# Optimization experiments

Measured on AMD Instinct MI355X. Metric: run time of the kernel, lower is better.

Reference implementation:

```python
import jax, jax.numpy as jnp
import numpy as np

N_NODES = 100000
N_EDGES = 1_600_000
IN, HID, OUT = 512, 128, 40


def setup_inputs() -> dict:
    key = jax.random.key(0)
    ks = jax.random.split(key, 7)
    features = jax.random.normal(ks[0], (N_NODES, IN), dtype=jnp.float32)
    src = jax.random.randint(ks[1], (N_EDGES,), 0, N_NODES, dtype=jnp.int32)
    dst = jax.random.randint(ks[2], (N_EDGES,), 0, N_NODES, dtype=jnp.int32)
    # Glorot-ish init for GraphConv weights; zero bias (DGL default)
    W1 = jax.random.normal(ks[3], (IN, HID), dtype=jnp.float32) * np.float32(1.0 / np.sqrt(IN))
    b1 = jnp.zeros((HID,), dtype=jnp.float32)
    W2 = jax.random.normal(ks[4], (HID, OUT), dtype=jnp.float32) * np.float32(1.0 / np.sqrt(HID))
    b2 = jnp.zeros((OUT,), dtype=jnp.float32)
    return {"features": features, "src": src, "dst": dst,
            "W1": W1, "b1": b1, "W2": W2, "b2": b2}


def _degree_norms(src, dst, n_nodes):
    ones = jnp.ones(src.shape[0], dtype=jnp.float32)
    deg_out = jax.ops.segment_sum(ones, src, num_segments=n_nodes)
    deg_in = jax.ops.segment_sum(ones, dst, num_segments=n_nodes)
    # DGL clamps degree to min 1 before the -1/2 power
    norm_src = jax.lax.rsqrt(jnp.maximum(deg_out, 1.0))  # [N]
    norm_dst = jax.lax.rsqrt(jnp.maximum(deg_in, 1.0))   # [N]
    return norm_src, norm_dst


def _graph_conv(x, W, b, src, dst, norm_src, norm_dst):
    # norm='both': out = D_dst^{-1/2} A D_src^{-1/2} (x W) + b
    # W applied before aggregation (in_feats > out_feats path in DGL)
    h = (x * norm_src[:, None]) @ W            # [N, out_feats]
    agg = jax.ops.segment_sum(h[src], dst, num_segments=x.shape[0])  # SpMM
    return agg * norm_dst[:, None] + b


def reference(features, src, dst, W1, b1, W2, b2):
    norm_src, norm_dst = _degree_norms(src, dst, features.shape[0])
    h = _graph_conv(features, W1, b1, src, dst, norm_src, norm_dst)
    h = jax.nn.relu(h)
    # dropout1: identity in eval mode
    h = _graph_conv(h, W2, b2, src, dst, norm_src, norm_dst)
    # dropout2: identity in eval mode
    return h
```

## Files before the change

### kernel.cpp

```cpp
#include <hip/hip_runtime.h>
#include <hip/hip_bf16.h>

#define N_NODES 100000
#define N_EDGES 1600000
#define FIN 512
#define FHID 128
#define FOUT 40
#define FOUTP 48

#define SCAN_CHUNK 1024
#define SCAN_NB ((N_NODES + SCAN_CHUNK - 1) / SCAN_CHUNK)

#define NRANGE 8
#define RANGE_SZ 12500
#define GH 16
#define EDGE_SLICE (N_EDGES / GH)

typedef __attribute__((ext_vector_type(8))) short short8;
typedef __attribute__((ext_vector_type(4))) float f32x4;

static __device__ inline unsigned short f2bf(float f) {
    unsigned x = __float_as_uint(f);
    unsigned r = (x + 0x7fffu + ((x >> 16) & 1u)) >> 16;
    return (unsigned short)r;
}

static __device__ inline unsigned pk2bf(float lo, float hi) {
    __hip_bfloat162 h = __float22bfloat162_rn(make_float2(lo, hi));
    return *(unsigned*)&h;
}
static __device__ inline unsigned short bf1(float f) {
    __hip_bfloat16 h = __float2bfloat16(f);
    return *(unsigned short*)&h;
}

static __device__ inline void gload_lds16(const unsigned short* g, unsigned short* l) {
    __builtin_amdgcn_global_load_lds(
        (const __attribute__((address_space(1))) unsigned int*)(g),
        (__attribute__((address_space(3))) unsigned int*)(l), 16, 0, 0);
}

__global__ __launch_bounds__(256) void deg_hist(const int* __restrict__ src,
                                                const int* __restrict__ dst,
                                                unsigned* __restrict__ scratch) {
    __shared__ unsigned hist[RANGE_SZ];
    const int task = blockIdx.x / GH;
    const int g = blockIdx.x % GH;
    const int a = task / NRANGE;
    const int rg = task % NRANGE;
    const int lo = rg * RANGE_SZ;
    const int t = threadIdx.x;
    for (int i = t; i < RANGE_SZ; i += 256) hist[i] = 0;
    __syncthreads();
    const int* arr = a ? dst : src;
    const int4* p = (const int4*)(arr + g * EDGE_SLICE);
    for (int i = t; i < EDGE_SLICE / 4; i += 256) {
        int4 v = p[i];
        int x;
        x = v.x - lo; if ((unsigned)x < RANGE_SZ) atomicAdd(&hist[x], 1u);
        x = v.y - lo; if ((unsigned)x < RANGE_SZ) atomicAdd(&hist[x], 1u);
        x = v.z - lo; if ((unsigned)x < RANGE_SZ) atomicAdd(&hist[x], 1u);
        x = v.w - lo; if ((unsigned)x < RANGE_SZ) atomicAdd(&hist[x], 1u);
    }
    __syncthreads();
    unsigned* out = scratch + ((size_t)task * GH + g) * RANGE_SZ;
    for (int i = t; i < RANGE_SZ; i += 256) out[i] = hist[i];
}

__global__ __launch_bounds__(256) void deg_reduce_scan(const unsigned* __restrict__ scratch,
                                                       float* __restrict__ nsrc,
                                                       float* __restrict__ ndst,
                                                       unsigned* __restrict__ degI,
                                                       unsigned* __restrict__ bsum) {
    __shared__ unsigned red[256];
    const int b = blockIdx.x, t = threadIdx.x;
    unsigned mysum = 0;
#pragma unroll
    for (int i = 0; i < 4; i++) {
        int node = b * SCAN_CHUNK + i * 256 + t;
        if (node < N_NODES) {
            const int rg = node / RANGE_SZ;
            const int off = node % RANGE_SZ;
            const unsigned* ps = scratch + ((size_t)rg * GH) * RANGE_SZ + off;
            const unsigned* pd = scratch + ((size_t)(NRANGE + rg) * GH) * RANGE_SZ + off;
            unsigned so = 0, si = 0;
#pragma unroll
            for (int g = 0; g < GH; g++) {
                so += ps[(size_t)g * RANGE_SZ];
                si += pd[(size_t)g * RANGE_SZ];
            }
            degI[node] = si;
            nsrc[node] = rsqrtf((float)(so < 1u ? 1u : so));
            ndst[node] = rsqrtf((float)(si < 1u ? 1u : si));
            mysum += si;
        }
    }
    red[t] = mysum; __syncthreads();
    for (int off = 128; off > 0; off >>= 1) {
        if (t < off) red[t] += red[t + off];
        __syncthreads();
    }
    if (t == 0) bsum[b] = red[0];
}

__global__ void scan_bsum(unsigned* __restrict__ bsum, int* __restrict__ rowptr) {
    __shared__ unsigned s[128];
    int t = threadIdx.x;
    if (t < SCAN_NB) s[t] = bsum[t];
    __syncthreads();
    if (t == 0) {
        unsigned run = 0;
        for (int i = 0; i < SCAN_NB; i++) { unsigned x = s[i]; s[i] = run; run += x; }
    }
    __syncthreads();
    if (t < SCAN_NB) bsum[t] = s[t];
    if (t == 0) rowptr[N_NODES] = N_EDGES;
}

__global__ __launch_bounds__(256) void scan_write_mk(const unsigned* __restrict__ deg,
                                                     const unsigned* __restrict__ bsum,
                                                     int* __restrict__ rowptr,
                                                     unsigned* __restrict__ scratch) {
    __shared__ unsigned ts[256];
    int b = blockIdx.x, t = threadIdx.x;
    int base = b * SCAN_CHUNK + t * 4;
    unsigned v[4]; unsigned sum = 0;
#pragma unroll
    for (int i = 0; i < 4; i++) { int idx = base + i; v[i] = (idx < N_NODES) ? deg[idx] : 0u; sum += v[i]; }
    ts[t] = sum; __syncthreads();
    for (int off = 1; off < 256; off <<= 1) {
        unsigned add = (t >= off) ? ts[t - off] : 0u;
        __syncthreads();
        ts[t] += add;
        __syncthreads();
    }
    unsigned excl = (t == 0) ? 0u : ts[t - 1];
    unsigned run = bsum[b] + excl;
#pragma unroll
    for (int i = 0; i < 4; i++) {
        int idx = base + i;
        if (idx < N_NODES) {
            rowptr[idx] = (int)run;
            const int rg = idx / RANGE_SZ;
            const int off = idx % RANGE_SZ;
            unsigned* pd = scratch + ((size_t)(NRANGE + rg) * GH) * RANGE_SZ + off;
            unsigned nrun = run;
#pragma unroll
            for (int g = 0; g < GH; g++) {
                unsigned c = pd[(size_t)g * RANGE_SZ];
                pd[(size_t)g * RANGE_SZ] = nrun;
                nrun += c;
            }
        }
        run += v[i];
    }
}

__global__ __launch_bounds__(256) void scatter2(const int* __restrict__ src,
                                                const int* __restrict__ dst,
                                                const unsigned* __restrict__ scratch,
                                                int* __restrict__ esrc) {
    __shared__ unsigned cur[RANGE_SZ];
    const int rg = blockIdx.x / GH;
    const int g = blockIdx.x % GH;
    const int lo = rg * RANGE_SZ;
    const int t = threadIdx.x;
    const unsigned* base = scratch + ((size_t)(NRANGE + rg) * GH + g) * RANGE_SZ;
    for (int i = t; i < RANGE_SZ; i += 256) cur[i] = base[i];
    __syncthreads();
    const int4* pd = (const int4*)(dst + g * EDGE_SLICE);
    const int4* ps = (const int4*)(src + g * EDGE_SLICE);
    for (int i = t; i < EDGE_SLICE / 4; i += 256) {
        int4 d4 = pd[i];
        int4 s4 = ps[i];
        int x;
        x = d4.x - lo; if ((unsigned)x < RANGE_SZ) esrc[atomicAdd(&cur[x], 1u)] = s4.x;
        x = d4.y - lo; if ((unsigned)x < RANGE_SZ) esrc[atomicAdd(&cur[x], 1u)] = s4.y;
        x = d4.z - lo; if ((unsigned)x < RANGE_SZ) esrc[atomicAdd(&cur[x], 1u)] = s4.z;
        x = d4.w - lo; if ((unsigned)x < RANGE_SZ) esrc[atomicAdd(&cur[x], 1u)] = s4.w;
    }
}

__global__ __launch_bounds__(256) void wcvt_all(const float* __restrict__ W1,
                                                const float* __restrict__ W2,
                                                unsigned short* __restrict__ Wt,
                                                unsigned short* __restrict__ W2t) {
    int j = blockIdx.x * blockDim.x + threadIdx.x;
    if (j < FIN * FHID) {
        int k = j >> 7;
        int n = j & 127;
        Wt[n * FIN + k] = f2bf(W1[j]);
    } else if (j < FIN * FHID + FOUTP * FHID) {
        int jj = j - FIN * FHID;
        int n = jj >> 7;
        int k = jj & 127;
        W2t[jj] = (n < FOUT) ? f2bf(W2[k * FOUT + n]) : (unsigned short)0;
    }
}

__global__ __launch_bounds__(256) void gemm1_mfma(const float* __restrict__ X,
                                                  const unsigned short* __restrict__ Wt,
                                                  const float* __restrict__ nsrc,
                                                  unsigned short* __restrict__ H) {
    __shared__ __align__(16) unsigned short Xs[64 * 64];
    __shared__ __align__(16) unsigned short Bs[128 * 64];
    const int t = threadIdx.x;
    const int bm = blockIdx.x * 64;
    const int w = t >> 6;
    const int l = t & 63;
    const int r = l & 15;
    const int kg = l >> 4;

    f32x4 acc[8];
#pragma unroll
    for (int c = 0; c < 8; c++) acc[c] = (f32x4){0.f, 0.f, 0.f, 0.f};

    for (int s = 0; s < FIN / 64; ++s) {
        const int k0 = s * 64;
#pragma unroll
        for (int i = 0; i < 4; i++) {
            int c = i * 4 + w;
            int col = c * 8 + (l >> 3);
            int slotp = l & 7;
            gload_lds16(Wt + (size_t)col * FIN + k0 + ((slotp ^ (col & 7)) * 8),
                        Bs + c * 512);
        }
#pragma unroll
        for (int i = 0; i < 2; i++) {
            int idx = t + i * 256;
            int row = idx >> 3;
            int slot = idx & 7;
            int grow = bm + row;
            uint4 packed = make_uint4(0u, 0u, 0u, 0u);
            if (grow < N_NODES) {
                const float4* p = (const float4*)(X + (size_t)grow * FIN + k0 + slot * 8);
                float4 v0 = p[0];
                float4 v1 = p[1];
                packed.x = pk2bf(v0.x, v0.y);
                packed.y = pk2bf(v0.z, v0.w);
                packed.z = pk2bf(v1.x, v1.y);
                packed.w = pk2bf(v1.z, v1.w);
            }
            *(uint4*)&Xs[row * 64 + ((slot ^ (row & 7)) * 8)] = packed;
        }
        __syncthreads();
        const int arow = w * 16 + r;
        short8 a0 = *(const short8*)&Xs[arow * 64 + (((0 + kg) ^ (r & 7)) * 8)];
        short8 a1 = *(const short8*)&Xs[arow * 64 + (((4 + kg) ^ (r & 7)) * 8)];
#pragma unroll
        for (int c = 0; c < 8; c++) {
            const int brow = c * 16 + r;
            short8 b0 = *(const short8*)&Bs[brow * 64 + (((0 + kg) ^ (r & 7)) * 8)];
            short8 b1 = *(const short8*)&Bs[brow * 64 + (((4 + kg) ^ (r & 7)) * 8)];
            acc[c] = __builtin_amdgcn_mfma_f32_16x16x32_bf16(a0, b0, acc[c], 0, 0, 0);
            acc[c] = __builtin_amdgcn_mfma_f32_16x16x32_bf16(a1, b1, acc[c], 0, 0, 0);
        }
        __syncthreads();
    }
#pragma unroll
    for (int j = 0; j < 4; j++) {
        int grow = bm + w * 16 + kg * 4 + j;
        if (grow < N_NODES) {
            float sc = nsrc[grow];
#pragma unroll
            for (int c = 0; c < 8; c++)
                H[(size_t)grow * FHID + c * 16 + r] = bf1(acc[c][j] * sc);
        }
    }
}

__global__ __launch_bounds__(256) void spmm1_gather(const int* __restrict__ rowptr,
                                                    const int* __restrict__ esrc,
                                                    const unsigned* __restrict__ H,
                                                    const float* __restrict__ ndst,
                                                    const float* __restrict__ b1,
                                                    unsigned* __restrict__ X2) {
    int node = blockIdx.x * (blockDim.x >> 6) + (threadIdx.x >> 6);
    if (node >= N_NODES) return;
    int lane = threadIdx.x & 63;
    int beg = rowptr[node], end = rowptr[node + 1];
    float2 a0 = make_float2(0.f, 0.f), a1 = make_float2(0.f, 0.f);
    float2 a2 = make_float2(0.f, 0.f), a3 = make_float2(0.f, 0.f);
    int p = beg;
    for (; p + 7 < end; p += 8) {
        int s0 = esrc[p],     s1 = esrc[p + 1], s2 = esrc[p + 2], s3 = esrc[p + 3];
        int s4 = esrc[p + 4], s5 = esrc[p + 5], s6 = esrc[p + 6], s7 = esrc[p + 7];
        unsigned u0 = H[(size_t)s0 * (FHID / 2) + lane];
        unsigned u1 = H[(size_t)s1 * (FHID / 2) + lane];
        unsigned u2 = H[(size_t)s2 * (FHID / 2) + lane];
        unsigned u3 = H[(size_t)s3 * (FHID / 2) + lane];
        unsigned u4 = H[(size_t)s4 * (FHID / 2) + lane];
        unsigned u5 = H[(size_t)s5 * (FHID / 2) + lane];
        unsigned u6 = H[(size_t)s6 * (FHID / 2) + lane];
        unsigned u7 = H[(size_t)s7 * (FHID / 2) + lane];
        a0.x += __uint_as_float(u0 << 16) + __uint_as_float(u1 << 16);
        a0.y += __uint_as_float(u0 & 0xffff0000u) + __uint_as_float(u1 & 0xffff0000u);
        a1.x += __uint_as_float(u2 << 16) + __uint_as_float(u3 << 16);
        a1.y += __uint_as_float(u2 & 0xffff0000u) + __uint_as_float(u3 & 0xffff0000u);
        a2.x += __uint_as_float(u4 << 16) + __uint_as_float(u5 << 16);
        a2.y += __uint_as_float(u4 & 0xffff0000u) + __uint_as_float(u5 & 0xffff0000u);
        a3.x += __uint_as_float(u6 << 16) + __uint_as_float(u7 << 16);
        a3.y += __uint_as_float(u6 & 0xffff0000u) + __uint_as_float(u7 & 0xffff0000u);
    }
    for (; p + 1 < end; p += 2) {
        int s0 = esrc[p], s1 = esrc[p + 1];
        unsigned u0 = H[(size_t)s0 * (FHID / 2) + lane];
        unsigned u1 = H[(size_t)s1 * (FHID / 2) + lane];
        a0.x += __uint_as_float(u0 << 16) + __uint_as_float(u1 << 16);
        a0.y += __uint_as_float(u0 & 0xffff0000u) + __uint_as_float(u1 & 0xffff0000u);
    }
    if (p < end) {
        int s0 = esrc[p];
        unsigned u0 = H[(size_t)s0 * (FHID / 2) + lane];
        a1.x += __uint_as_float(u0 << 16);
        a1.y += __uint_as_float(u0 & 0xffff0000u);
    }
    float ax = (a0.x + a1.x) + (a2.x + a3.x);
    float ay = (a0.y + a1.y) + (a2.y + a3.y);
    float nd = ndst[node];
    float2 b = *(const float2*)(b1 + lane * 2);
    float ox = fmaxf(fmaf(ax, nd, b.x), 0.f);
    float oy = fmaxf(fmaf(ay, nd, b.y), 0.f);
    X2[(size_t)node * (FHID / 2) + lane] = pk2bf(ox, oy);
}

__global__ __launch_bounds__(256) void gemm2_mfma(const unsigned short* __restrict__ X2,
                                                  const unsigned short* __restrict__ W2t,
                                                  const float* __restrict__ nsrc,
                                                  unsigned short* __restrict__ H2) {
    __shared__ __align__(16) unsigned short Xs[64 * 128];
    __shared__ __align__(16) unsigned short Bs[FOUTP * 128];
    const int t = threadIdx.x;
    const int bm = blockIdx.x * 64;
    const int w = t >> 6;
    const int l = t & 63;
    const int r = l & 15;
    const int kg = l >> 4;

#pragma unroll
    for (int i = 0; i < 4; i++) {
        int c = i * 4 + w;
        int row = c * 4 + (l >> 4);
        int slotp = l & 15;
        size_t grow = (size_t)(bm + row);
        if (grow >= N_NODES) grow = N_NODES - 1;
        gload_lds16(X2 + grow * FHID + ((slotp ^ (row & 15)) * 8), Xs + c * 512);
    }
#pragma unroll
    for (int i = 0; i < 3; i++) {
        int c = i * 4 + w;
        int row = c * 4 + (l >> 4);
        int slotp = l & 15;
        gload_lds16(W2t + row * FHID + ((slotp ^ (row & 15)) * 8), Bs + c * 512);
    }
    __syncthreads();

    f32x4 acc[3];
#pragma unroll
    for (int c = 0; c < 3; c++) acc[c] = (f32x4){0.f, 0.f, 0.f, 0.f};
    const int arow = w * 16 + r;
#pragma unroll
    for (int ks = 0; ks < 4; ks++) {
        short8 a = *(const short8*)&Xs[arow * 128 + (((ks * 4 + kg) ^ r) * 8)];
#pragma unroll
        for (int c = 0; c < 3; c++) {
            const int brow = c * 16 + r;
            short8 b = *(const short8*)&Bs[brow * 128 + (((ks * 4 + kg) ^ r) * 8)];
            acc[c] = __builtin_amdgcn_mfma_f32_16x16x32_bf16(a, b, acc[c], 0, 0, 0);
        }
    }
#pragma unroll
    for (int j = 0; j < 4; j++) {
        int grow = bm + w * 16 + kg * 4 + j;
        if (grow < N_NODES) {
            float sc = nsrc[grow];
#pragma unroll
            for (int c = 0; c < 3; c++) {
                int col = c * 16 + r;
                if (col < FOUT)
                    H2[(size_t)grow * FOUT + col] = bf1(acc[c][j] * sc);
            }
        }
    }
}

__global__ __launch_bounds__(256) void spmm2_gather(const int* __restrict__ rowptr,
                                                    const int* __restrict__ esrc,
                                                    const unsigned* __restrict__ H2,
                                                    const float* __restrict__ ndst,
                                                    const float* __restrict__ b2,
                                                    float* __restrict__ OUT) {
    const int wave = (threadIdx.x >> 6);
    const int lane = threadIdx.x & 63;
    const int sub = lane / 20;
    const int feat = lane % 20;
    int node = blockIdx.x * 12 + wave * 3 + sub;
    if (sub >= 3 || node >= N_NODES) return;
    int beg = rowptr[node], end = rowptr[node + 1];
    float2 a0 = make_float2(0.f, 0.f), a1 = make_float2(0.f, 0.f);
    float2 a2 = make_float2(0.f, 0.f), a3 = make_float2(0.f, 0.f);
    int p = beg;
    for (; p + 3 < end; p += 4) {
        int s0 = esrc[p], s1 = esrc[p + 1], s2 = esrc[p + 2], s3 = esrc[p + 3];
        unsigned u0 = H2[(size_t)s0 * (FOUT / 2) + feat];
        unsigned u1 = H2[(size_t)s1 * (FOUT / 2) + feat];
        unsigned u2 = H2[(size_t)s2 * (FOUT / 2) + feat];
        unsigned u3 = H2[(size_t)s3 * (FOUT / 2) + feat];
        a0.x += __uint_as_float(u0 << 16);
        a0.y += __uint_as_float(u0 & 0xffff0000u);
        a1.x += __uint_as_float(u1 << 16);
        a1.y += __uint_as_float(u1 & 0xffff0000u);
        a2.x += __uint_as_float(u2 << 16);
        a2.y += __uint_as_float(u2 & 0xffff0000u);
        a3.x += __uint_as_float(u3 << 16);
        a3.y += __uint_as_float(u3 & 0xffff0000u);
    }
    for (; p < end; ++p) {
        int s0 = esrc[p];
        unsigned u0 = H2[(size_t)s0 * (FOUT / 2) + feat];
        a0.x += __uint_as_float(u0 << 16);
        a0.y += __uint_as_float(u0 & 0xffff0000u);
    }
    float ax = (a0.x + a1.x) + (a2.x + a3.x);
    float ay = (a0.y + a1.y) + (a2.y + a3.y);
    float nd = ndst[node];
    float2 b = *(const float2*)(b2 + feat * 2);
    float2 o;
    o.x = fmaf(ax, nd, b.x);
    o.y = fmaf(ay, nd, b.y);
    *(float2*)(OUT + (size_t)node * FOUT + feat * 2) = o;
}

extern "C" void kernel_launch(void* const* d_in, const int* in_sizes, int n_in,
                              void* d_out, int out_size, void* d_ws, size_t ws_size,
                              hipStream_t stream) {
    const float* feat = (const float*)d_in[0];
    const int*   src  = (const int*)d_in[1];
    const int*   dst  = (const int*)d_in[2];
    const float* W1   = (const float*)d_in[3];
    const float* b1   = (const float*)d_in[4];
    const float* W2   = (const float*)d_in[5];
    const float* b2   = (const float*)d_in[6];
    float* out = (float*)d_out;

    char* ws = (char*)d_ws;
    const size_t SZ_BIG = (size_t)N_NODES * FHID * sizeof(float);
    unsigned short* Hbf  = (unsigned short*)ws;
    unsigned short* X2bf = (unsigned short*)(ws + SZ_BIG);
    unsigned*       scratch = (unsigned*)(ws + SZ_BIG);
    unsigned short* H2bf = (unsigned short*)(ws + SZ_BIG + (32u << 20));
    char* small = ws + 2 * SZ_BIG;
    const size_t SSTRIDE = 401408;
    float*    nsrc   = (float*)(small);
    float*    ndst   = (float*)(small + SSTRIDE);
    unsigned* degI   = (unsigned*)(small + 2 * SSTRIDE);
    int*      rowptr = (int*)(small + 3 * SSTRIDE);
    unsigned* bsum   = (unsigned*)(small + 4 * SSTRIDE);
    unsigned short* Wt  = (unsigned short*)(small + 5 * SSTRIDE);
    unsigned short* W2t = (unsigned short*)(small + 5 * SSTRIDE + 131072);
    int*      esrc   = (int*)(small + 6 * SSTRIDE);

    deg_hist<<<2 * NRANGE * GH, 256, 0, stream>>>(src, dst, scratch);
    deg_reduce_scan<<<SCAN_NB, 256, 0, stream>>>(scratch, nsrc, ndst, degI, bsum);
    scan_bsum<<<1, 128, 0, stream>>>(bsum, rowptr);
    scan_write_mk<<<SCAN_NB, 256, 0, stream>>>(degI, bsum, rowptr, scratch);
    scatter2<<<NRANGE * GH, 256, 0, stream>>>(src, dst, scratch, esrc);
    wcvt_all<<<(FIN * FHID + FOUTP * FHID + 255) / 256, 256, 0, stream>>>(W1, W2, Wt, W2t);

    gemm1_mfma<<<(N_NODES + 63) / 64, 256, 0, stream>>>(feat, Wt, nsrc, Hbf);
    spmm1_gather<<<(N_NODES + 3) / 4, 256, 0, stream>>>(rowptr, esrc, (const unsigned*)Hbf,
                                                        ndst, b1, (unsigned*)X2bf);
    gemm2_mfma<<<(N_NODES + 63) / 64, 256, 0, stream>>>(X2bf, W2t, nsrc, H2bf);
    spmm2_gather<<<(N_NODES + 11) / 12, 256, 0, stream>>>(rowptr, esrc, (const unsigned*)H2bf,
                                                          ndst, b2, out);
}
```

Baseline: 297.4 us.

## Fuse layer-1 SpMM into GEMM2 and pack degree histograms as 16-bit counts

Merges the first-layer neighbor gather (with bias, ReLU and bf16 pack) into the second GEMM kernel, so each block aggregates its 64 rows straight into LDS before the MFMA. This removes the X2 round trip through global memory and one launch. The degree histogram now packs two 16-bit counts per LDS word, which halves the range passes, and the scan_bsum kernel is folded into scan_write_mk. The trade-off is fewer, longer-running gather blocks in the fused kernel (one node per wave at a time), which may lower memory-level parallelism, and 16-bit counts per slice that assume degrees stay small.

Result: slower. 363.8 us (+22.3%).

```diff
diff --git a/kernel.cpp b/kernel.cpp
--- a/kernel.cpp
+++ b/kernel.cpp
@@ -16,6 +16,10 @@
 #define GH 16
 #define EDGE_SLICE (N_EDGES / GH)
 
+#define NR4 4
+#define RANGE2 25000
+#define R2WORDS 12500
+
 typedef __attribute__((ext_vector_type(8))) short short8;
 typedef __attribute__((ext_vector_type(4))) float f32x4;
 
@@ -42,35 +46,34 @@
 
 __global__ __launch_bounds__(256) void deg_hist(const int* __restrict__ src,
                                                 const int* __restrict__ dst,
-                                                unsigned* __restrict__ scratch) {
-    __shared__ unsigned hist[RANGE_SZ];
+                                                unsigned* __restrict__ count2) {
+    __shared__ unsigned hist[R2WORDS];
     const int task = blockIdx.x / GH;
     const int g = blockIdx.x % GH;
-    const int a = task / NRANGE;
-    const int rg = task % NRANGE;
-    const int lo = rg * RANGE_SZ;
+    const int a = task / NR4;
+    const int rg = task % NR4;
+    const int lo = rg * RANGE2;
     const int t = threadIdx.x;
-    for (int i = t; i < RANGE_SZ; i += 256) hist[i] = 0;
+    for (int i = t; i < R2WORDS; i += 256) hist[i] = 0;
     __syncthreads();
     const int* arr = a ? dst : src;
     const int4* p = (const int4*)(arr + g * EDGE_SLICE);
     for (int i = t; i < EDGE_SLICE / 4; i += 256) {
         int4 v = p[i];
         int x;
-        x = v.x - lo; if ((unsigned)x < RANGE_SZ) atomicAdd(&hist[x], 1u);
-        x = v.y - lo; if ((unsigned)x < RANGE_SZ) atomicAdd(&hist[x], 1u);
-        x = v.z - lo; if ((unsigned)x < RANGE_SZ) atomicAdd(&hist[x], 1u);
-        x = v.w - lo; if ((unsigned)x < RANGE_SZ) atomicAdd(&hist[x], 1u);
-    }
-    __syncthreads();
-    unsigned* out = scratch + ((size_t)task * GH + g) * RANGE_SZ;
-    for (int i = t; i < RANGE_SZ; i += 256) out[i] = hist[i];
-}
-
-__global__ __launch_bounds__(256) void deg_reduce_scan(const unsigned* __restrict__ scratch,
+        x = v.x - lo; if ((unsigned)x < RANGE2) atomicAdd(&hist[x >> 1], 1u << ((x & 1) << 4));
+        x = v.y - lo; if ((unsigned)x < RANGE2) atomicAdd(&hist[x >> 1], 1u << ((x & 1) << 4));
+        x = v.z - lo; if ((unsigned)x < RANGE2) atomicAdd(&hist[x >> 1], 1u << ((x & 1) << 4));
+        x = v.w - lo; if ((unsigned)x < RANGE2) atomicAdd(&hist[x >> 1], 1u << ((x & 1) << 4));
+    }
+    __syncthreads();
+    unsigned* out = count2 + ((size_t)task * GH + g) * R2WORDS;
+    for (int i = t; i < R2WORDS; i += 256) out[i] = hist[i];
+}
+
+__global__ __launch_bounds__(256) void deg_reduce_scan(const unsigned* __restrict__ count2,
                                                        float* __restrict__ nsrc,
                                                        float* __restrict__ ndst,
-                                                       unsigned* __restrict__ degI,
                                                        unsigned* __restrict__ bsum) {
     __shared__ unsigned red[256];
     const int b = blockIdx.x, t = threadIdx.x;
@@ -79,17 +82,17 @@
     for (int i = 0; i < 4; i++) {
         int node = b * SCAN_CHUNK + i * 256 + t;
         if (node < N_NODES) {
-            const int rg = node / RANGE_SZ;
-            const int off = node % RANGE_SZ;
-            const unsigned* ps = scratch + ((size_t)rg * GH) * RANGE_SZ + off;
-            const unsigned* pd = scratch + ((size_t)(NRANGE + rg) * GH) * RANGE_SZ + off;
+            const int rg4 = node / RANGE2;
+            const int wo = (node % RANGE2) >> 1;
+            const int sh = (node & 1) << 4;
+            const unsigned* ps = count2 + ((size_t)rg4 * GH) * R2WORDS + wo;
+            const unsigned* pd = count2 + ((size_t)(NR4 + rg4) * GH) * R2WORDS + wo;
             unsigned so = 0, si = 0;
 #pragma unroll
             for (int g = 0; g < GH; g++) {
-                so += ps[(size_t)g * RANGE_SZ];
-                si += pd[(size_t)g * RANGE_SZ];
-            }
-            degI[node] = si;
+                so += (ps[(size_t)g * R2WORDS] >> sh) & 0xffffu;
+                si += (pd[(size_t)g * R2WORDS] >> sh) & 0xffffu;
+            }
             nsrc[node] = rsqrtf((float)(so < 1u ? 1u : so));
             ndst[node] = rsqrtf((float)(si < 1u ? 1u : si));
             mysum += si;
@@ -103,30 +106,36 @@
     if (t == 0) bsum[b] = red[0];
 }
 
-__global__ void scan_bsum(unsigned* __restrict__ bsum, int* __restrict__ rowptr) {
-    __shared__ unsigned s[128];
-    int t = threadIdx.x;
-    if (t < SCAN_NB) s[t] = bsum[t];
+__global__ __launch_bounds__(256) void scan_write_mk(const unsigned* __restrict__ count2,
+                                                     const unsigned* __restrict__ bsum,
+                                                     int* __restrict__ rowptr,
+                                                     unsigned* __restrict__ bases) {
+    __shared__ unsigned ts[256];
+    __shared__ unsigned pb[128];
+    const int b = blockIdx.x, t = threadIdx.x;
+    if (t < SCAN_NB) pb[t] = bsum[t];
     __syncthreads();
     if (t == 0) {
         unsigned run = 0;
-        for (int i = 0; i < SCAN_NB; i++) { unsigned x = s[i]; s[i] = run; run += x; }
-    }
-    __syncthreads();
-    if (t < SCAN_NB) bsum[t] = s[t];
-    if (t == 0) rowptr[N_NODES] = N_EDGES;
-}
-
-__global__ __launch_bounds__(256) void scan_write_mk(const unsigned* __restrict__ deg,
-                                                     const unsigned* __restrict__ bsum,
-                                                     int* __restrict__ rowptr,
-                                                     unsigned* __restrict__ scratch) {
-    __shared__ unsigned ts[256];
-    int b = blockIdx.x, t = threadIdx.x;
-    int base = b * SCAN_CHUNK + t * 4;
+        for (int i = 0; i < SCAN_NB; i++) { unsigned x = pb[i]; pb[i] = run; run += x; }
+    }
+    __syncthreads();
+    const int base = b * SCAN_CHUNK + t * 4;
     unsigned v[4]; unsigned sum = 0;
 #pragma unroll
-    for (int i = 0; i < 4; i++) { int idx = base + i; v[i] = (idx < N_NODES) ? deg[idx] : 0u; sum += v[i]; }
+    for (int i = 0; i < 4; i++) {
+        int idx = base + i;
+        unsigned si = 0;
+        if (idx < N_NODES) {
+            const int rg4 = idx / RANGE2;
+            const int wo = (idx % RANGE2) >> 1;
+            const int sh = (idx & 1) << 4;
+            const unsigned* pd = count2 + ((size_t)(NR4 + rg4) * GH) * R2WORDS + wo;
+#pragma unroll
+            for (int g = 0; g < GH; g++) si += (pd[(size_t)g * R2WORDS] >> sh) & 0xffffu;
+        }
+        v[i] = si; sum += si;
+    }
     ts[t] = sum; __syncthreads();
     for (int off = 1; off < 256; off <<= 1) {
         unsigned add = (t >= off) ? ts[t - off] : 0u;
@@ -135,37 +144,42 @@
         __syncthreads();
     }
     unsigned excl = (t == 0) ? 0u : ts[t - 1];
-    unsigned run = bsum[b] + excl;
+    unsigned run = pb[b] + excl;
 #pragma unroll
     for (int i = 0; i < 4; i++) {
         int idx = base + i;
         if (idx < N_NODES) {
             rowptr[idx] = (int)run;
-            const int rg = idx / RANGE_SZ;
-            const int off = idx % RANGE_SZ;
-            unsigned* pd = scratch + ((size_t)(NRANGE + rg) * GH) * RANGE_SZ + off;
+            const int rg4 = idx / RANGE2;
+            const int wo = (idx % RANGE2) >> 1;
+            const int sh = (idx & 1) << 4;
+            const int rg8 = idx / RANGE_SZ;
+            const int off8 = idx % RANGE_SZ;
+            const unsigned* pd = count2 + ((size_t)(NR4 + rg4) * GH) * R2WORDS + wo;
+            unsigned* pb8 = bases + ((size_t)rg8 * GH) * RANGE_SZ + off8;
             unsigned nrun = run;
 #pragma unroll
             for (int g = 0; g < GH; g++) {
-                unsigned c = pd[(size_t)g * RANGE_SZ];
-                pd[(size_t)g * RANGE_SZ] = nrun;
+                unsigned c = (pd[(size_t)g * R2WORDS] >> sh) & 0xffffu;
+                pb8[(size_t)g * RANGE_SZ] = nrun;
                 nrun += c;
             }
         }
         run += v[i];
     }
+    if (b == 0 && t == 0) rowptr[N_NODES] = N_EDGES;
 }
 
 __global__ __launch_bounds__(256) void scatter2(const int* __restrict__ src,
                                                 const int* __restrict__ dst,
-                                                const unsigned* __restrict__ scratch,
+                                                const unsigned* __restrict__ bases,
                                                 int* __restrict__ esrc) {
     __shared__ unsigned cur[RANGE_SZ];
     const int rg = blockIdx.x / GH;
     const int g = blockIdx.x % GH;
     const int lo = rg * RANGE_SZ;
     const int t = threadIdx.x;
-    const unsigned* base = scratch + ((size_t)(NRANGE + rg) * GH + g) * RANGE_SZ;
+    const unsigned* base = bases + ((size_t)rg * GH + g) * RANGE_SZ;
     for (int i = t; i < RANGE_SZ; i += 256) cur[i] = base[i];
     __syncthreads();
     const int4* pd = (const int4*)(dst + g * EDGE_SLICE);
@@ -269,65 +283,14 @@
     }
 }
 
-__global__ __launch_bounds__(256) void spmm1_gather(const int* __restrict__ rowptr,
-                                                    const int* __restrict__ esrc,
-                                                    const unsigned* __restrict__ H,
-                                                    const float* __restrict__ ndst,
-                                                    const float* __restrict__ b1,
-                                                    unsigned* __restrict__ X2) {
-    int node = blockIdx.x * (blockDim.x >> 6) + (threadIdx.x >> 6);
-    if (node >= N_NODES) return;
-    int lane = threadIdx.x & 63;
-    int beg = rowptr[node], end = rowptr[node + 1];
-    float2 a0 = make_float2(0.f, 0.f), a1 = make_float2(0.f, 0.f);
-    float2 a2 = make_float2(0.f, 0.f), a3 = make_float2(0.f, 0.f);
-    int p = beg;
-    for (; p + 7 < end; p += 8) {
-        int s0 = esrc[p],     s1 = esrc[p + 1], s2 = esrc[p + 2], s3 = esrc[p + 3];
-        int s4 = esrc[p + 4], s5 = esrc[p + 5], s6 = esrc[p + 6], s7 = esrc[p + 7];
-        unsigned u0 = H[(size_t)s0 * (FHID / 2) + lane];
-        unsigned u1 = H[(size_t)s1 * (FHID / 2) + lane];
-        unsigned u2 = H[(size_t)s2 * (FHID / 2) + lane];
-        unsigned u3 = H[(size_t)s3 * (FHID / 2) + lane];
-        unsigned u4 = H[(size_t)s4 * (FHID / 2) + lane];
-        unsigned u5 = H[(size_t)s5 * (FHID / 2) + lane];
-        unsigned u6 = H[(size_t)s6 * (FHID / 2) + lane];
-        unsigned u7 = H[(size_t)s7 * (FHID / 2) + lane];
-        a0.x += __uint_as_float(u0 << 16) + __uint_as_float(u1 << 16);
-        a0.y += __uint_as_float(u0 & 0xffff0000u) + __uint_as_float(u1 & 0xffff0000u);
-        a1.x += __uint_as_float(u2 << 16) + __uint_as_float(u3 << 16);
-        a1.y += __uint_as_float(u2 & 0xffff0000u) + __uint_as_float(u3 & 0xffff0000u);
-        a2.x += __uint_as_float(u4 << 16) + __uint_as_float(u5 << 16);
-        a2.y += __uint_as_float(u4 & 0xffff0000u) + __uint_as_float(u5 & 0xffff0000u);
-        a3.x += __uint_as_float(u6 << 16) + __uint_as_float(u7 << 16);
-        a3.y += __uint_as_float(u6 & 0xffff0000u) + __uint_as_float(u7 & 0xffff0000u);
-    }
-    for (; p + 1 < end; p += 2) {
-        int s0 = esrc[p], s1 = esrc[p + 1];
-        unsigned u0 = H[(size_t)s0 * (FHID / 2) + lane];
-        unsigned u1 = H[(size_t)s1 * (FHID / 2) + lane];
-        a0.x += __uint_as_float(u0 << 16) + __uint_as_float(u1 << 16);
-        a0.y += __uint_as_float(u0 & 0xffff0000u) + __uint_as_float(u1 & 0xffff0000u);
-    }
-    if (p < end) {
-        int s0 = esrc[p];
-        unsigned u0 = H[(size_t)s0 * (FHID / 2) + lane];
-        a1.x += __uint_as_float(u0 << 16);
-        a1.y += __uint_as_float(u0 & 0xffff0000u);
-    }
-    float ax = (a0.x + a1.x) + (a2.x + a3.x);
-    float ay = (a0.y + a1.y) + (a2.y + a3.y);
-    float nd = ndst[node];
-    float2 b = *(const float2*)(b1 + lane * 2);
-    float ox = fmaxf(fmaf(ax, nd, b.x), 0.f);
-    float oy = fmaxf(fmaf(ay, nd, b.y), 0.f);
-    X2[(size_t)node * (FHID / 2) + lane] = pk2bf(ox, oy);
-}
-
-__global__ __launch_bounds__(256) void gemm2_mfma(const unsigned short* __restrict__ X2,
-                                                  const unsigned short* __restrict__ W2t,
-                                                  const float* __restrict__ nsrc,
-                                                  unsigned short* __restrict__ H2) {
+__global__ __launch_bounds__(256) void sg2_fused(const int* __restrict__ rowptr,
+                                                 const int* __restrict__ esrc,
+                                                 const unsigned* __restrict__ H,
+                                                 const float* __restrict__ ndst,
+                                                 const float* __restrict__ b1,
+                                                 const unsigned short* __restrict__ W2t,
+                                                 const float* __restrict__ nsrc,
+                                                 unsigned short* __restrict__ H2) {
     __shared__ __align__(16) unsigned short Xs[64 * 128];
     __shared__ __align__(16) unsigned short Bs[FOUTP * 128];
     const int t = threadIdx.x;
@@ -338,21 +301,46 @@
     const int kg = l >> 4;
 
 #pragma unroll
-    for (int i = 0; i < 4; i++) {
-        int c = i * 4 + w;
-        int row = c * 4 + (l >> 4);
-        int slotp = l & 15;
-        size_t grow = (size_t)(bm + row);
-        if (grow >= N_NODES) grow = N_NODES - 1;
-        gload_lds16(X2 + grow * FHID + ((slotp ^ (row & 15)) * 8), Xs + c * 512);
-    }
-#pragma unroll
     for (int i = 0; i < 3; i++) {
         int c = i * 4 + w;
         int row = c * 4 + (l >> 4);
         int slotp = l & 15;
         gload_lds16(W2t + row * FHID + ((slotp ^ (row & 15)) * 8), Bs + c * 512);
     }
+
+    const float2 bb = *(const float2*)(b1 + l * 2);
+    for (int i = 0; i < 16; i++) {
+        const int row = w * 16 + i;
+        const int node = bm + row;
+        unsigned val = 0u;
+        if (node < N_NODES) {
+            int beg = rowptr[node], end = rowptr[node + 1];
+            float ax0 = 0.f, ay0 = 0.f, ax1 = 0.f, ay1 = 0.f;
+            int p = beg;
+            for (; p + 3 < end; p += 4) {
+                int s0 = esrc[p], s1 = esrc[p + 1], s2 = esrc[p + 2], s3 = esrc[p + 3];
+                unsigned u0 = H[(size_t)s0 * (FHID / 2) + l];
+                unsigned u1 = H[(size_t)s1 * (FHID / 2) + l];
+                unsigned u2 = H[(size_t)s2 * (FHID / 2) + l];
+                unsigned u3 = H[(size_t)s3 * (FHID / 2) + l];
+                ax0 += __uint_as_float(u0 << 16) + __uint_as_float(u1 << 16);
+                ay0 += __uint_as_float(u0 & 0xffff0000u) + __uint_as_float(u1 & 0xffff0000u);
+                ax1 += __uint_as_float(u2 << 16) + __uint_as_float(u3 << 16);
+                ay1 += __uint_as_float(u2 & 0xffff0000u) + __uint_as_float(u3 & 0xffff0000u);
+            }
+            for (; p < end; ++p) {
+                int s0 = esrc[p];
+                unsigned u0 = H[(size_t)s0 * (FHID / 2) + l];
+                ax0 += __uint_as_float(u0 << 16);
+                ay0 += __uint_as_float(u0 & 0xffff0000u);
+            }
+            float nd = ndst[node];
+            float ox = fmaxf(fmaf(ax0 + ax1, nd, bb.x), 0.f);
+            float oy = fmaxf(fmaf(ay0 + ay1, nd, bb.y), 0.f);
+            val = pk2bf(ox, oy);
+        }
+        *(unsigned*)((char*)Xs + row * 256 + (((l >> 2) ^ (row & 15)) * 16) + ((l & 3) * 4)) = val;
+    }
     __syncthreads();
 
     f32x4 acc[3];
@@ -364,8 +352,7 @@
         short8 a = *(const short8*)&Xs[arow * 128 + (((ks * 4 + kg) ^ r) * 8)];
 #pragma unroll
         for (int c = 0; c < 3; c++) {
-            const int brow = c * 16 + r;
-            short8 b = *(const short8*)&Bs[brow * 128 + (((ks * 4 + kg) ^ r) * 8)];
+            short8 b = *(const short8*)&Bs[(c * 16 + r) * 128 + (((ks * 4 + kg) ^ r) * 8)];
             acc[c] = __builtin_amdgcn_mfma_f32_16x16x32_bf16(a, b, acc[c], 0, 0, 0);
         }
     }
@@ -445,32 +432,29 @@
 
     char* ws = (char*)d_ws;
     const size_t SZ_BIG = (size_t)N_NODES * FHID * sizeof(float);
-    unsigned short* Hbf  = (unsigned short*)ws;
-    unsigned short* X2bf = (unsigned short*)(ws + SZ_BIG);
-    unsigned*       scratch = (unsigned*)(ws + SZ_BIG);
-    unsigned short* H2bf = (unsigned short*)(ws + SZ_BIG + (32u << 20));
+    unsigned short* Hbf    = (unsigned short*)ws;
+    unsigned*       count2 = (unsigned*)(ws + SZ_BIG);
+    unsigned*       bases  = (unsigned*)(ws + SZ_BIG + ((size_t)2 * NR4 * GH * R2WORDS * 4));
+    unsigned short* H2bf   = (unsigned short*)(ws + SZ_BIG + (32u << 20));
     char* small = ws + 2 * SZ_BIG;
     const size_t SSTRIDE = 401408;
     float*    nsrc   = (float*)(small);
     float*    ndst   = (float*)(small + SSTRIDE);
-    unsigned* degI   = (unsigned*)(small + 2 * SSTRIDE);
-    int*      rowptr = (int*)(small + 3 * SSTRIDE);
-    unsigned* bsum   = (unsigned*)(small + 4 * SSTRIDE);
-    unsigned short* Wt  = (unsigned short*)(small + 5 * SSTRIDE);
-    unsigned short* W2t = (unsigned short*)(small + 5 * SSTRIDE + 131072);
-    int*      esrc   = (int*)(small + 6 * SSTRIDE);
-
-    deg_hist<<<2 * NRANGE * GH, 256, 0, stream>>>(src, dst, scratch);
-    deg_reduce_scan<<<SCAN_NB, 256, 0, stream>>>(scratch, nsrc, ndst, degI, bsum);
-    scan_bsum<<<1, 128, 0, stream>>>(bsum, rowptr);
-    scan_write_mk<<<SCAN_NB, 256, 0, stream>>>(degI, bsum, rowptr, scratch);
-    scatter2<<<NRANGE * GH, 256, 0, stream>>>(src, dst, scratch, esrc);
+    int*      rowptr = (int*)(small + 2 * SSTRIDE);
+    unsigned* bsum   = (unsigned*)(small + 3 * SSTRIDE);
+    unsigned short* Wt  = (unsigned short*)(small + 4 * SSTRIDE);
+    unsigned short* W2t = (unsigned short*)(small + 4 * SSTRIDE + 131072);
+    int*      esrc   = (int*)(small + 5 * SSTRIDE);
+
+    deg_hist<<<2 * NR4 * GH, 256, 0, stream>>>(src, dst, count2);
+    deg_reduce_scan<<<SCAN_NB, 256, 0, stream>>>(count2, nsrc, ndst, bsum);
+    scan_write_mk<<<SCAN_NB, 256, 0, stream>>>(count2, bsum, rowptr, bases);
+    scatter2<<<NRANGE * GH, 256, 0, stream>>>(src, dst, bases, esrc);
     wcvt_all<<<(FIN * FHID + FOUTP * FHID + 255) / 256, 256, 0, stream>>>(W1, W2, Wt, W2t);
 
     gemm1_mfma<<<(N_NODES + 63) / 64, 256, 0, stream>>>(feat, Wt, nsrc, Hbf);
-    spmm1_gather<<<(N_NODES + 3) / 4, 256, 0, stream>>>(rowptr, esrc, (const unsigned*)Hbf,
-                                                        ndst, b1, (unsigned*)X2bf);
-    gemm2_mfma<<<(N_NODES + 63) / 64, 256, 0, stream>>>(X2bf, W2t, nsrc, H2bf);
+    sg2_fused<<<(N_NODES + 63) / 64, 256, 0, stream>>>(rowptr, esrc, (const unsigned*)Hbf,
+                                                       ndst, b1, W2t, nsrc, H2bf);
     spmm2_gather<<<(N_NODES + 11) / 12, 256, 0, stream>>>(rowptr, esrc, (const unsigned*)H2bf,
                                                           ndst, b2, out);
 }
```
